# Kernel optimization log

Hardware: AMD Instinct MI355X
Metric: run time of the kernel (lower is better)

## Reference

```python
import jax, jax.numpy as jnp
import numpy as np

TOP_K = 8
N_EXPERTS = 64
HIDDEN = 4096


def setup_inputs() -> dict:
    key = jax.random.key(0)
    k1, k2 = jax.random.split(key)
    hidden_states = jax.random.normal(k1, (4, 4096, HIDDEN), dtype=jnp.float32)
    # kaiming_uniform_(a=sqrt(5)) on a (64, 4096) weight -> U(-b, b), b = sqrt(6/((1+5)*4096)) = 1/sqrt(4096)
    bound = 1.0 / np.sqrt(HIDDEN)
    weight = jax.random.uniform(k2, (N_EXPERTS, HIDDEN), dtype=jnp.float32,
                                minval=-bound, maxval=bound)
    return {"hidden_states": hidden_states, "weight": weight}


def reference(hidden_states, weight):
    bsz, seq_len, h = hidden_states.shape
    x = hidden_states.reshape(-1, h)                       # [T, H]
    logits = jnp.einsum('th,eh->te', x, weight)            # [T, E]
    scores = jax.nn.softmax(logits, axis=-1)
    topk_weight, topk_idx = jax.lax.top_k(scores, TOP_K)   # [T, K]
    denom = jnp.sum(topk_weight, axis=-1, keepdims=True) + 1e-20
    topk_weight = topk_weight / denom
    topk_weight = topk_weight.reshape(bsz, seq_len, TOP_K)
    topk_idx = topk_idx.reshape(bsz, seq_len, TOP_K)
    # training-time aux loss (seq_aux path): histogram of argmax expert * mean prob
    probs = scores                                         # softmax(logits)
    top1 = jnp.argmax(probs, axis=-1)                      # [T]
    counts = jnp.zeros((N_EXPERTS,), dtype=jnp.float32).at[top1].add(1.0)
    route_prob = jnp.mean(probs, axis=0)                   # [E]
    route_frac = counts / jnp.sum(counts)
    aux_loss = jnp.sum(route_prob * route_frac) * N_EXPERTS
    return topk_idx, topk_weight, aux_loss
```

## Files before the change

### kernel.cpp

```cpp
#include <hip/hip_runtime.h>
#include <hip/hip_bf16.h>

#define TOKS 16384
#define HID  4096
#define NEXP 64
#define EPS  1e-4f

#define WS_FLAGCNT  128
#define WS_FLAGLIST 192
#define WS_BPACK    16576
#define BPK_LO      262144

typedef __attribute__((ext_vector_type(8))) short short8_t;
typedef __attribute__((ext_vector_type(4))) float f32x4;

static __device__ __forceinline__ unsigned short f2bf_rn(float x) {
    unsigned u = __builtin_bit_cast(unsigned, x);
    u = (u + 0x7fffu + ((u >> 16) & 1u)) >> 16;
    return (unsigned short)u;
}
static __device__ __forceinline__ float bf2f(unsigned short h) {
    return __builtin_bit_cast(float, (unsigned)h << 16);
}

__global__ void moe_prep(const float* __restrict__ W, unsigned short* __restrict__ Bpk,
                         float* __restrict__ wsf) {
    const int idx = blockIdx.x * blockDim.x + threadIdx.x;
    if (idx < 192) wsf[idx] = 0.0f;
    if (idx >= NEXP * HID) return;
    const int n = idx >> 12;
    const int k = idx & 4095;
    const float w = W[idx];
    const unsigned short hi = f2bf_rn(w);
    const unsigned short lo = f2bf_rn(w - bf2f(hi));
    const int kt   = k >> 5;
    const int nt   = n >> 4;
    const int lane = (n & 15) | (((k >> 3) & 3) << 4);
    const int j    = k & 7;
    const int dst  = (((kt << 2) + nt) << 9) + (lane << 3) + j;
    Bpk[dst]          = hi;
    Bpk[BPK_LO + dst] = lo;
}

__global__ __launch_bounds__(256, 4)
void moe_fused(const float* __restrict__ X, const unsigned short* __restrict__ Bpk,
               float* __restrict__ out, float* __restrict__ wsf) {
    __shared__ __align__(16) float L[4][16][68];

    const int tid  = threadIdx.x;
    const int lane = tid & 63;
    const int w    = tid >> 6;
    const int tok0 = blockIdx.x * 16;

    const int mrow = lane & 15;
    const int g    = lane >> 4;
    const size_t xbase = (size_t)(tok0 + mrow) * HID + ((size_t)w << 10) + (g << 3);
    const unsigned short* bb0 = Bpk + (((size_t)w << 5) << 11) + (lane << 3);

    f32x4 acc[4];
    #pragma unroll
    for (int nt = 0; nt < 4; ++nt) acc[nt] = (f32x4){0.f, 0.f, 0.f, 0.f};

    #pragma unroll 2
    for (int c = 0; c < 32; ++c) {
        const float4 xa = *(const float4*)&X[xbase + (c << 5)];
        const float4 xb = *(const float4*)&X[xbase + (c << 5) + 4];
        const float xv[8] = {xa.x, xa.y, xa.z, xa.w, xb.x, xb.y, xb.z, xb.w};
        short8_t ah, al;
        #pragma unroll
        for (int j = 0; j < 8; ++j) {
            const unsigned short h = f2bf_rn(xv[j]);
            ah[j] = (short)h;
            al[j] = (short)f2bf_rn(xv[j] - bf2f(h));
        }
        const unsigned short* bb = bb0 + ((size_t)c << 11);
        #pragma unroll
        for (int nt = 0; nt < 4; ++nt) {
            const short8_t bh = *(const short8_t*)(bb + (nt << 9));
            const short8_t bl = *(const short8_t*)(bb + BPK_LO + (nt << 9));
            acc[nt] = __builtin_amdgcn_mfma_f32_16x16x32_bf16(ah, bh, acc[nt], 0, 0, 0);
            acc[nt] = __builtin_amdgcn_mfma_f32_16x16x32_bf16(al, bh, acc[nt], 0, 0, 0);
            acc[nt] = __builtin_amdgcn_mfma_f32_16x16x32_bf16(ah, bl, acc[nt], 0, 0, 0);
        }
    }

    #pragma unroll
    for (int nt = 0; nt < 4; ++nt)
        #pragma unroll
        for (int r = 0; r < 4; ++r)
            L[w][(g << 2) + r][(nt << 4) + mrow] = acc[nt][r];
    __syncthreads();

    float* outIdx = out;
    float* outW   = out + TOKS * 8;
    int* flagcnt  = (int*)wsf + WS_FLAGCNT;
    int* flaglist = (int*)wsf + WS_FLAGLIST;

    float rp = 0.f;
    #pragma unroll
    for (int tt = 0; tt < 4; ++tt) {
        const int tl = (w << 2) + tt;
        const float lg = (L[0][tl][lane] + L[1][tl][lane]) + (L[2][tl][lane] + L[3][tl][lane]);

        float v = lg; int idx = lane;
        #pragma unroll
        for (int size = 2; size <= 64; size <<= 1) {
            #pragma unroll
            for (int str = size >> 1; str > 0; str >>= 1) {
                const float ov = __shfl_xor(v, str, 64);
                const int   oi = __shfl_xor(idx, str, 64);
                const bool pb = (ov > v) || (ov == v && oi < idx);
                const bool keepFirst = ((lane & str) == 0) == ((lane & size) == 0);
                if (pb == keepFirst) { v = ov; idx = oi; }
            }
        }

        const float m = __shfl(v, 0, 64);
        const float p = __expf(lg - m);
        float s = p;
        #pragma unroll
        for (int o = 32; o; o >>= 1) s += __shfl_xor(s, o, 64);
        const float inv_s = 1.0f / s;
        rp += p * inv_s;

        const float wkv = __expf(v - m) * inv_s;
        float d8 = (lane < 8) ? wkv : 0.f;
        #pragma unroll
        for (int o = 1; o < 8; o <<= 1) d8 += __shfl_xor(d8, o, 64);
        const float invd = 1.0f / (d8 + 1e-20f);
        const float nv = __shfl_down(v, 1, 64);
        const bool flg = __any(lane < 8 && (v - nv) < EPS);

        const int gtok = tok0 + tl;
        if (lane < 8) {
            outIdx[(size_t)gtok * 8 + lane] = (float)idx;
            outW[(size_t)gtok * 8 + lane]   = wkv * invd;
        }
        if (lane == 0) {
            atomicAdd(&wsf[NEXP + idx], 1.0f);
            if (flg) {
                const int pos = atomicAdd(flagcnt, 1);
                if (pos < TOKS) flaglist[pos] = gtok;
            }
        }
    }
    atomicAdd(&wsf[lane], rp);
}

__global__ __launch_bounds__(256, 2)
void moe_fix(const float* __restrict__ X, const float* __restrict__ W,
             float* __restrict__ out, float* __restrict__ wsf) {
    __shared__ double red[256];
    const int tid = threadIdx.x;
    const int e   = tid & 63;
    const int kc  = tid >> 6;
    const int nf  = min(*((int*)wsf + WS_FLAGCNT), TOKS);
    const int* flaglist = (const int*)wsf + WS_FLAGLIST;
    float* outIdx = out;
    float* outW   = out + TOKS * 8;

    for (int fi = blockIdx.x; fi < nf; fi += gridDim.x) {
        const int tok = flaglist[fi];
        const float* xrow = X + (size_t)tok * HID + kc * 1024;
        const float* wrow = W + (size_t)e  * HID + kc * 1024;
        double part = 0.0;
        for (int j = 0; j < 1024; j += 4) {
            const float4 xv = *(const float4*)(xrow + j);
            const float4 wv = *(const float4*)(wrow + j);
            part = fma((double)xv.x, (double)wv.x, part);
            part = fma((double)xv.y, (double)wv.y, part);
            part = fma((double)xv.z, (double)wv.z, part);
            part = fma((double)xv.w, (double)wv.w, part);
        }
        red[tid] = part;
        __syncthreads();
        if (tid < 64) {
            const double lg = ((red[tid] + red[64 + tid]) + red[128 + tid]) + red[192 + tid];
            const float lgf = (float)lg;
            float m = lgf;
            #pragma unroll
            for (int o = 32; o; o >>= 1) m = fmaxf(m, __shfl_xor(m, o, 64));
            const float p = __expf(lgf - m);
            float s = p;
            #pragma unroll
            for (int o = 32; o; o >>= 1) s += __shfl_xor(s, o, 64);
            const float inv_s = 1.0f / s;

            double v = lg;
            double bw[8]; int ik[8];
            #pragma unroll
            for (int k = 0; k < 8; ++k) {
                double bv = v; int bi = tid;
                #pragma unroll
                for (int o = 32; o; o >>= 1) {
                    const double ov = __shfl_xor(bv, o, 64);
                    const int    oi = __shfl_xor(bi, o, 64);
                    if (ov > bv || (ov == bv && oi < bi)) { bv = ov; bi = oi; }
                }
                bw[k] = bv; ik[k] = bi;
                if (tid == bi) v = -1.0e300;
            }
            float wk[8]; float denom = 1e-20f;
            #pragma unroll
            for (int k = 0; k < 8; ++k) {
                wk[k] = __expf((float)bw[k] - m) * inv_s; denom += wk[k];
            }
            const float invd = 1.0f / denom;
            const size_t base = (size_t)tok * 8;
            const int oldtop = (int)outIdx[base];
            if (tid < 8) {
                outIdx[base + tid] = (float)ik[tid];
                outW[base + tid]   = wk[tid] * invd;
            }
            if (tid == 0 && ik[0] != oldtop) {
                atomicAdd(&wsf[NEXP + oldtop], -1.0f);
                atomicAdd(&wsf[NEXP + ik[0]],  1.0f);
            }
        }
        __syncthreads();
    }
}

__global__ void moe_final(const float* __restrict__ wsf, float* __restrict__ out) {
    const int e = threadIdx.x;
    float v = wsf[e] * wsf[NEXP + e];
    #pragma unroll
    for (int o = 32; o; o >>= 1) v += __shfl_xor(v, o, 64);
    if (e == 0)
        out[2 * TOKS * 8] = v * (64.0f / ((float)TOKS * (float)TOKS));
}

__global__ void moe_init(float* __restrict__ wsf, int n) {
    const int i = blockIdx.x * blockDim.x + threadIdx.x;
    if (i < n) wsf[i] = 0.0f;
}

__global__ void moe_w_cvt(const float* __restrict__ W, double* __restrict__ Wd) {
    const int i = blockIdx.x * blockDim.x + threadIdx.x;
    if (i < NEXP * HID) Wd[i] = (double)W[i];
}

__global__ __launch_bounds__(512, 2)
void moe_mono(const float* __restrict__ X, const double* __restrict__ Wd,
              float* __restrict__ out, float* __restrict__ wsf) {
    __shared__ double xs[64][66];
    __shared__ double L2[64][65];
    const int tid  = threadIdx.x;
    const int lane = tid & 63;
    const int wid  = __builtin_amdgcn_readfirstlane(tid >> 6);
    const int tok0 = blockIdx.x * 64;
    double acc[8] = {0., 0., 0., 0., 0., 0., 0., 0.};
    for (int h0 = 0; h0 < HID; h0 += 64) {
        #pragma unroll
        for (int i = 0; i < 8; ++i) {
            const int li = tid + i * 512;
            xs[li >> 6][li & 63] = (double)X[((size_t)(tok0 + (li >> 6)) << 12) + (h0 + (li & 63))];
        }
        __syncthreads();
        const double* wchunk = Wd + (((size_t)(wid << 3)) << 12) + h0;
        #pragma unroll 2
        for (int hh = 0; hh < 64; hh += 2) {
            const double2 xv = *(const double2*)&xs[lane][hh];
            #pragma unroll
            for (int e = 0; e < 8; ++e) {
                const double* wr = wchunk + (((size_t)e) << 12) + hh;
                acc[e] = fma(xv.x, wr[0], acc[e]);
                acc[e] = fma(xv.y, wr[1], acc[e]);
            }
        }
        __syncthreads();
    }
    #pragma unroll
    for (int e = 0; e < 8; ++e) L2[lane][(wid << 3) + e] = acc[e];
    __syncthreads();
    float* outIdx = out;
    float* outW   = out + (TOKS * 8);
    float rp = 0.0f;
    for (int tt = 0; tt < 8; ++tt) {
        const int t = (wid << 3) + tt;
        const double lg = L2[t][lane];
        const float lgf = (float)lg;
        float m = lgf;
        #pragma unroll
        for (int o = 32; o; o >>= 1) m = fmaxf(m, __shfl_xor(m, o, 64));
        const float p = __expf(lgf - m);
        float s = p;
        #pragma unroll
        for (int o = 32; o; o >>= 1) s += __shfl_xor(s, o, 64);
        const float inv_s = 1.0f / s;
        rp += p * inv_s;
        double v = lg;
        float wk[8]; int ik[8];
        #pragma unroll
        for (int k = 0; k < 8; ++k) {
            double bv = v; int bi = lane;
            #pragma unroll
            for (int o = 32; o; o >>= 1) {
                const double ov = __shfl_xor(bv, o, 64);
                const int    oi = __shfl_xor(bi, o, 64);
                if (ov > bv || (ov == bv && oi < bi)) { bv = ov; bi = oi; }
            }
            wk[k] = __expf((float)bv - m) * inv_s; ik[k] = bi;
            if (lane == bi) v = -1.0e300;
        }
        if (lane == 0) {
            const float denom = (((wk[0]+wk[1])+(wk[2]+wk[3])) +
                                 ((wk[4]+wk[5])+(wk[6]+wk[7]))) + 1e-20f;
            const float invd = 1.0f / denom;
            const size_t base = ((size_t)(tok0 + t)) << 3;
            #pragma unroll
            for (int k = 0; k < 8; ++k) {
                outIdx[base + k] = (float)ik[k];
                outW[base + k]   = wk[k] * invd;
            }
            atomicAdd(&wsf[NEXP + ik[0]], 1.0f);
        }
    }
    atomicAdd(&wsf[lane], rp);
}

extern "C" void kernel_launch(void* const* d_in, const int* in_sizes, int n_in,
                              void* d_out, int out_size, void* d_ws, size_t ws_size,
                              hipStream_t stream) {
    const float* X = (const float*)d_in[0];
    const float* W = (const float*)d_in[1];
    float* out = (float*)d_out;
    float* wsf = (float*)d_ws;

    const size_t need = 4ull * WS_BPACK + 4ull * BPK_LO;

    if (ws_size >= need) {
        unsigned short* Bpk = (unsigned short*)(wsf + WS_BPACK);
        moe_prep<<<(NEXP * HID + 255) / 256, 256, 0, stream>>>(W, Bpk, wsf);
        moe_fused<<<TOKS / 16, 256, 0, stream>>>(X, Bpk, out, wsf);
        moe_fix<<<256, 256, 0, stream>>>(X, W, out, wsf);
        moe_final<<<1, 64, 0, stream>>>(wsf, out);
    } else {
        double* Wd = (double*)d_ws;
        float* wsf2 = (float*)(Wd + NEXP * HID);
        moe_w_cvt<<<(NEXP * HID + 255) / 256, 256, 0, stream>>>(W, Wd);
        moe_init<<<1, 256, 0, stream>>>(wsf2, 128);
        moe_mono<<<TOKS / 64, 512, 0, stream>>>(X, Wd, out, wsf2);
        moe_final<<<1, 64, 0, stream>>>(wsf2, out);
    }
}
```

Before: 239.8 us.

## Tile router GEMM 64 tokens per block with double-buffered LDS staging

The fused router GEMM now processes 64 tokens per 512-thread block instead of 16 per 256-thread block. X and the packed hi/lo bf16 weights are staged into double-buffered LDS with global_load_lds, and the X tiles use an XOR swizzle. The weight layout interleaves hi and lo halves so each k-tile is contiguous. This reuses each weight tile across 64 tokens, cutting global weight traffic, and overlaps loads with MFMA work, at the cost of more LDS, a barrier every k-step and fewer tokens of split-K parallelism per wave.

```diff
diff --git a/kernel.cpp b/kernel.cpp
--- a/kernel.cpp
+++ b/kernel.cpp
@@ -9,7 +9,6 @@
 #define WS_FLAGCNT  128
 #define WS_FLAGLIST 192
 #define WS_BPACK    16576
-#define BPK_LO      262144
 
 typedef __attribute__((ext_vector_type(8))) short short8_t;
 typedef __attribute__((ext_vector_type(4))) float f32x4;
@@ -21,6 +20,11 @@
 }
 static __device__ __forceinline__ float bf2f(unsigned short h) {
     return __builtin_bit_cast(float, (unsigned)h << 16);
+}
+static __device__ __forceinline__ void gl2lds16(const void* g, void* l) {
+    __builtin_amdgcn_global_load_lds(
+        (const __attribute__((address_space(1))) unsigned int*)g,
+        (__attribute__((address_space(3))) unsigned int*)l, 16, 0, 0);
 }
 
 __global__ void moe_prep(const float* __restrict__ W, unsigned short* __restrict__ Bpk,
@@ -37,58 +41,92 @@
     const int nt   = n >> 4;
     const int lane = (n & 15) | (((k >> 3) & 3) << 4);
     const int j    = k & 7;
-    const int dst  = (((kt << 2) + nt) << 9) + (lane << 3) + j;
-    Bpk[dst]          = hi;
-    Bpk[BPK_LO + dst] = lo;
-}
-
-__global__ __launch_bounds__(256, 4)
+    const int dst  = (((kt << 2) + nt) << 10) + (lane << 3) + j;
+    Bpk[dst]       = hi;
+    Bpk[dst + 512] = lo;
+}
+
+__global__ __launch_bounds__(512, 2)
 void moe_fused(const float* __restrict__ X, const unsigned short* __restrict__ Bpk,
                float* __restrict__ out, float* __restrict__ wsf) {
-    __shared__ __align__(16) float L[4][16][68];
+    __shared__ __align__(16) float xbuf[2][64][64];
+    __shared__ __align__(16) unsigned short bbuf[2][8192];
+    float (*L)[68] = (float (*)[68])&xbuf[0][0][0];
 
     const int tid  = threadIdx.x;
     const int lane = tid & 63;
     const int w    = tid >> 6;
-    const int tok0 = blockIdx.x * 16;
-
-    const int mrow = lane & 15;
+    const int mt   = w & 3;
+    const int nh   = w >> 2;
     const int g    = lane >> 4;
-    const size_t xbase = (size_t)(tok0 + mrow) * HID + ((size_t)w << 10) + (g << 3);
-    const unsigned short* bb0 = Bpk + (((size_t)w << 5) << 11) + (lane << 3);
-
-    f32x4 acc[4];
+    const int tok0 = blockIdx.x * 64;
+
+    f32x4 acc[2];
+    acc[0] = (f32x4){0.f, 0.f, 0.f, 0.f};
+    acc[1] = (f32x4){0.f, 0.f, 0.f, 0.f};
+
+    #define STAGE(buf, s)                                                            \
+    {                                                                                \
+        const int k0_ = (s) << 6;                                                    \
+        _Pragma("unroll")                                                            \
+        for (int i = 0; i < 2; ++i) {                                                \
+            const int rg = (w << 3) + (i << 2) + g;                                  \
+            const int ck = (lane & 15) ^ (rg & 15);                                  \
+            gl2lds16(X + (size_t)(tok0 + rg) * HID + k0_ + (ck << 2),                \
+                     (void*)&xbuf[buf][(w << 3) + (i << 2)][0]);                     \
+        }                                                                            \
+        _Pragma("unroll")                                                            \
+        for (int j = 0; j < 2; ++j) {                                                \
+            const int c1k = (w << 1) + j;                                            \
+            gl2lds16((const char*)Bpk + ((size_t)(s) << 14) + (c1k << 10) + (lane << 4), \
+                     (void*)((char*)&bbuf[buf][0] + (c1k << 10)));                   \
+        }                                                                            \
+    }
+
+    STAGE(0, 0);
+    __syncthreads();
+
+    const int tr = (mt << 4) + (lane & 15);
+    const char* arow = (const char*)&xbuf[0][tr][0];
+    const int rsw = lane & 15;
+
+    for (int s = 0; s < 64; ++s) {
+        const int cur = s & 1;
+        if (s < 63) STAGE(cur ^ 1, s + 1);
+
+        const char* ab = arow + cur * 16384;
+        const char* bb = (const char*)&bbuf[cur][0];
+        #pragma unroll
+        for (int ktl = 0; ktl < 2; ++ktl) {
+            const int cl = (ktl << 3) + (g << 1);
+            const float4 a0 = *(const float4*)(ab + ((cl ^ rsw) << 4));
+            const float4 a1 = *(const float4*)(ab + (((cl + 1) ^ rsw) << 4));
+            const float xv[8] = {a0.x, a0.y, a0.z, a0.w, a1.x, a1.y, a1.z, a1.w};
+            short8_t ah, al;
+            #pragma unroll
+            for (int j = 0; j < 8; ++j) {
+                const unsigned short h = f2bf_rn(xv[j]);
+                ah[j] = (short)h;
+                al[j] = (short)f2bf_rn(xv[j] - bf2f(h));
+            }
+            #pragma unroll
+            for (int ntl = 0; ntl < 2; ++ntl) {
+                const char* bp = bb + (((ktl << 2) + (nh << 1) + ntl) << 11) + (lane << 4);
+                const short8_t bh = *(const short8_t*)bp;
+                const short8_t bl = *(const short8_t*)(bp + 1024);
+                acc[ntl] = __builtin_amdgcn_mfma_f32_16x16x32_bf16(ah, bh, acc[ntl], 0, 0, 0);
+                acc[ntl] = __builtin_amdgcn_mfma_f32_16x16x32_bf16(al, bh, acc[ntl], 0, 0, 0);
+                acc[ntl] = __builtin_amdgcn_mfma_f32_16x16x32_bf16(ah, bl, acc[ntl], 0, 0, 0);
+            }
+        }
+        __syncthreads();
+    }
+
     #pragma unroll
-    for (int nt = 0; nt < 4; ++nt) acc[nt] = (f32x4){0.f, 0.f, 0.f, 0.f};
-
-    #pragma unroll 2
-    for (int c = 0; c < 32; ++c) {
-        const float4 xa = *(const float4*)&X[xbase + (c << 5)];
-        const float4 xb = *(const float4*)&X[xbase + (c << 5) + 4];
-        const float xv[8] = {xa.x, xa.y, xa.z, xa.w, xb.x, xb.y, xb.z, xb.w};
-        short8_t ah, al;
-        #pragma unroll
-        for (int j = 0; j < 8; ++j) {
-            const unsigned short h = f2bf_rn(xv[j]);
-            ah[j] = (short)h;
-            al[j] = (short)f2bf_rn(xv[j] - bf2f(h));
-        }
-        const unsigned short* bb = bb0 + ((size_t)c << 11);
-        #pragma unroll
-        for (int nt = 0; nt < 4; ++nt) {
-            const short8_t bh = *(const short8_t*)(bb + (nt << 9));
-            const short8_t bl = *(const short8_t*)(bb + BPK_LO + (nt << 9));
-            acc[nt] = __builtin_amdgcn_mfma_f32_16x16x32_bf16(ah, bh, acc[nt], 0, 0, 0);
-            acc[nt] = __builtin_amdgcn_mfma_f32_16x16x32_bf16(al, bh, acc[nt], 0, 0, 0);
-            acc[nt] = __builtin_amdgcn_mfma_f32_16x16x32_bf16(ah, bl, acc[nt], 0, 0, 0);
-        }
-    }
-
-    #pragma unroll
-    for (int nt = 0; nt < 4; ++nt)
+    for (int ntl = 0; ntl < 2; ++ntl)
         #pragma unroll
         for (int r = 0; r < 4; ++r)
-            L[w][(g << 2) + r][(nt << 4) + mrow] = acc[nt][r];
+            L[(mt << 4) + (g << 2) + r][(nh << 5) + (ntl << 4) + (lane & 15)] = acc[ntl][r];
     __syncthreads();
 
     float* outIdx = out;
@@ -98,9 +136,9 @@
 
     float rp = 0.f;
     #pragma unroll
-    for (int tt = 0; tt < 4; ++tt) {
-        const int tl = (w << 2) + tt;
-        const float lg = (L[0][tl][lane] + L[1][tl][lane]) + (L[2][tl][lane] + L[3][tl][lane]);
+    for (int tt = 0; tt < 8; ++tt) {
+        const int tl = (w << 3) + tt;
+        const float lg = L[tl][lane];
 
         float v = lg; int idx = lane;
         #pragma unroll
@@ -117,10 +155,10 @@
 
         const float m = __shfl(v, 0, 64);
         const float p = __expf(lg - m);
-        float s = p;
-        #pragma unroll
-        for (int o = 32; o; o >>= 1) s += __shfl_xor(s, o, 64);
-        const float inv_s = 1.0f / s;
+        float sdenom = p;
+        #pragma unroll
+        for (int o = 32; o; o >>= 1) sdenom += __shfl_xor(sdenom, o, 64);
+        const float inv_s = 1.0f / sdenom;
         rp += p * inv_s;
 
         const float wkv = __expf(v - m) * inv_s;
@@ -145,6 +183,7 @@
         }
     }
     atomicAdd(&wsf[lane], rp);
+    #undef STAGE
 }
 
 __global__ __launch_bounds__(256, 2)
@@ -327,12 +366,12 @@
     float* out = (float*)d_out;
     float* wsf = (float*)d_ws;
 
-    const size_t need = 4ull * WS_BPACK + 4ull * BPK_LO;
+    const size_t need = 4ull * WS_BPACK + 2ull * 524288;
 
     if (ws_size >= need) {
         unsigned short* Bpk = (unsigned short*)(wsf + WS_BPACK);
         moe_prep<<<(NEXP * HID + 255) / 256, 256, 0, stream>>>(W, Bpk, wsf);
-        moe_fused<<<TOKS / 16, 256, 0, stream>>>(X, Bpk, out, wsf);
+        moe_fused<<<TOKS / 64, 512, 0, stream>>>(X, Bpk, out, wsf);
         moe_fix<<<256, 256, 0, stream>>>(X, W, out, wsf);
         moe_final<<<1, 64, 0, stream>>>(wsf, out);
     } else {
```

After: 236.8 us. About the same (-1.3%).
